# Performance work log

Hardware: AMD Instinct MI355X
Metric: run time of the kernel (lower is better)

Reference implementation:

```python
import jax, jax.numpy as jnp
import numpy as np

N_CARD = 100000
N_MERCH = 50000
E = 1000000
DIN = 64
H = 128


def setup_inputs() -> dict:
    key = jax.random.key(0)
    ks = iter(jax.random.split(key, 40))

    def nrm(shape, scale=0.05):
        return jax.random.normal(next(ks), shape, jnp.float32) * scale

    inp = {}
    inp["x_card"] = jax.random.normal(next(ks), (N_CARD, DIN), jnp.float32)
    inp["x_merchant"] = jax.random.normal(next(ks), (N_MERCH, DIN), jnp.float32)
    inp["src_cm"] = jax.random.randint(next(ks), (E,), 0, N_CARD, jnp.int32)
    inp["dst_cm"] = jax.random.randint(next(ks), (E,), 0, N_MERCH, jnp.int32)
    inp["src_mc"] = jax.random.randint(next(ks), (E,), 0, N_MERCH, jnp.int32)
    inp["dst_mc"] = jax.random.randint(next(ks), (E,), 0, N_CARD, jnp.int32)
    # SAGEConv weights per layer / edge type: lin_l (on aggregated msgs, with bias), lin_r (on dst, no bias)
    inp["Wl0_cm"] = nrm((DIN, H)); inp["bl0_cm"] = jnp.zeros((H,), jnp.float32); inp["Wr0_cm"] = nrm((DIN, H))
    inp["Wl0_mc"] = nrm((DIN, H)); inp["bl0_mc"] = jnp.zeros((H,), jnp.float32); inp["Wr0_mc"] = nrm((DIN, H))
    inp["Wl1_cm"] = nrm((H, H)); inp["bl1_cm"] = jnp.zeros((H,), jnp.float32); inp["Wr1_cm"] = nrm((H, H))
    inp["Wl1_mc"] = nrm((H, H)); inp["bl1_mc"] = jnp.zeros((H,), jnp.float32); inp["Wr1_mc"] = nrm((H, H))
    # per-node-type fraud classifiers: Linear(H, H//2) -> ReLU -> Linear(H//2, 2)
    inp["cW1_card"] = nrm((H, H // 2)); inp["cb1_card"] = jnp.zeros((H // 2,), jnp.float32)
    inp["cW2_card"] = nrm((H // 2, 2)); inp["cb2_card"] = jnp.zeros((2,), jnp.float32)
    inp["cW1_merch"] = nrm((H, H // 2)); inp["cb1_merch"] = jnp.zeros((H // 2,), jnp.float32)
    inp["cW2_merch"] = nrm((H // 2, 2)); inp["cb2_merch"] = jnp.zeros((2,), jnp.float32)
    # shared risk scorer: Linear(H, H//2) -> ReLU -> Linear(H//2, 1) -> sigmoid
    inp["rW1"] = nrm((H, H // 2)); inp["rb1"] = jnp.zeros((H // 2,), jnp.float32)
    inp["rW2"] = nrm((H // 2, 1)); inp["rb2"] = jnp.zeros((1,), jnp.float32)
    return inp


def _sage(x_src, x_dst, src, dst, Wl, bl, Wr, n_dst):
    # gather neighbor features, scatter-mean by destination, then lin_l + lin_r(x_dst)
    msg = x_src[src]                                           # [E, Din]
    agg = jax.ops.segment_sum(msg, dst, num_segments=n_dst)    # [n_dst, Din]
    cnt = jax.ops.segment_sum(jnp.ones((src.shape[0],), x_src.dtype), dst, num_segments=n_dst)
    mean = agg / jnp.maximum(cnt, 1.0)[:, None]
    return mean @ Wl + bl + x_dst @ Wr


def _mlp2(x, W1, b1, W2, b2):
    return jax.nn.relu(x @ W1 + b1) @ W2 + b2


def reference(x_card, x_merchant, src_cm, dst_cm, src_mc, dst_mc,
              Wl0_cm, bl0_cm, Wr0_cm, Wl0_mc, bl0_mc, Wr0_mc,
              Wl1_cm, bl1_cm, Wr1_cm, Wl1_mc, bl1_mc, Wr1_mc,
              cW1_card, cb1_card, cW2_card, cb2_card,
              cW1_merch, cb1_merch, cW2_merch, cb2_merch,
              rW1, rb1, rW2, rb2):
    # layer 0 (eval mode: dropout is identity)
    h_m = jax.nn.relu(_sage(x_card, x_merchant, src_cm, dst_cm, Wl0_cm, bl0_cm, Wr0_cm, N_MERCH))
    h_c = jax.nn.relu(_sage(x_merchant, x_card, src_mc, dst_mc, Wl0_mc, bl0_mc, Wr0_mc, N_CARD))
    # layer 1
    h_m2 = jax.nn.relu(_sage(h_c, h_m, src_cm, dst_cm, Wl1_cm, bl1_cm, Wr1_cm, N_MERCH))
    h_c2 = jax.nn.relu(_sage(h_m, h_c, src_mc, dst_mc, Wl1_mc, bl1_mc, Wr1_mc, N_CARD))
    # heads
    pred_c = _mlp2(h_c2, cW1_card, cb1_card, cW2_card, cb2_card)      # [N_CARD, 2]
    pred_m = _mlp2(h_m2, cW1_merch, cb1_merch, cW2_merch, cb2_merch)  # [N_MERCH, 2]
    risk_c = jax.nn.sigmoid(_mlp2(h_c2, rW1, rb1, rW2, rb2))[:, 0]    # [N_CARD]
    risk_m = jax.nn.sigmoid(_mlp2(h_m2, rW1, rb1, rW2, rb2))[:, 0]    # [N_MERCH]
    return (h_c2, h_m2, pred_c, pred_m, risk_c, risk_m)
```

## Files before the change

kernel.cpp:

```cpp
#include <hip/hip_runtime.h>


typedef unsigned short u16;
typedef unsigned int u32;
typedef short bf16x8 __attribute__((ext_vector_type(8)));
typedef float f32x4 __attribute__((ext_vector_type(4)));
typedef u16 u16x4 __attribute__((ext_vector_type(4)));
typedef u16 u16x8 __attribute__((ext_vector_type(8)));

#define CAP 64
#define LDS_PAD 8
#define NXCD 8
#define ECHUNK 64
#define NBUILD (NXCD * ECHUNK * 2)
#define NPACK  768

__device__ __forceinline__ float bf2f(u16 u) {
    union { u32 i; float f; } v; v.i = ((u32)u) << 16; return v.f;
}
__device__ __forceinline__ u16 f2bf(float f) {
    union { float f; u32 i; } v; v.f = f;
    u32 i = v.i;
    return (u16)((i + 0x7FFFu + ((i >> 16) & 1u)) >> 16);
}
__device__ __forceinline__ bf16x8 cvt8(const float* p) {
    bf16x8 r;
#pragma unroll
    for (int i = 0; i < 8; ++i) r[i] = (short)f2bf(p[i]);
    return r;
}

struct PackDesc { const float* src; u16* dst; int K; int Nsrc; int ntOff; };
struct PrepArgs {
    const int* src_cm; const int* dst_cm; const int* src_mc; const int* dst_mc;
    int* cnt_m; u32* bucket_m; int* cnt_c; u16* bucket_c;
    int E; int nMerch; int nCard;
    const float* xc; u16* xcb; int ncBlk;
    const float* xm; u16* xmb; int nmBlk;
    PackDesc pd[12];
};

__global__ void __launch_bounds__(256) prep(PrepArgs a) {
    const int b = blockIdx.x;
    if (b < NBUILD) {
        const int g = b & 7;
        const int chunk = (b >> 3) & 63;
        const bool dirA = b < (NBUILD / 2);
        const int nNode = dirA ? a.nMerch : a.nCard;
        const int lo = (int)((long long)g * nNode / NXCD);
        const int hi = (int)((long long)(g + 1) * nNode / NXCD);
        const int* dst = dirA ? a.dst_cm : a.dst_mc;
        const int* src = dirA ? a.src_cm : a.src_mc;
        int* cnt = dirA ? a.cnt_m : a.cnt_c;
        const int e0 = (int)((long long)chunk * a.E / ECHUNK);
        const int e1 = (int)((long long)(chunk + 1) * a.E / ECHUNK);
        for (int i = e0 + threadIdx.x; i < e1; i += 256) {
            int d = __builtin_nontemporal_load(dst + i);
            if (d >= lo && d < hi) {
                int slot = atomicAdd(&cnt[d], 1);
                if (slot < CAP) {
                    int s = __builtin_nontemporal_load(src + i);
                    if (dirA) a.bucket_m[(size_t)d * CAP + slot] = (u32)s;
                    else      a.bucket_c[(size_t)d * CAP + slot] = (u16)s;
                }
            }
        }
    } else if (b < NBUILD + NPACK) {
        int e = b - NBUILD;
        PackDesc pd = a.pd[e >> 6];
        int idx = (e & 63) * 256 + threadIdx.x;
        int j = idx & 7;
        int lane = (idx >> 3) & 63;
        int t = idx >> 9;
        int nLocal = pd.Nsrc >> 4;
        int ntl = t % nLocal;
        int kt = t / nLocal;
        if (kt >= (pd.K >> 5)) return;
        int k = kt * 32 + ((lane >> 4) << 3) + j;
        int n = ntl * 16 + (lane & 15);
        pd.dst[(((kt * 8 + pd.ntOff + ntl) * 64) + lane) * 8 + j] = f2bf(pd.src[k * pd.Nsrc + n]);
    } else {
        int e = b - NBUILD - NPACK;
        const float* s;
        u16* d;
        int n;
        if (e < a.ncBlk) { s = a.xc; d = a.xcb; n = a.nCard * 64; }
        else             { e -= a.ncBlk; s = a.xm; d = a.xmb; n = a.nMerch * 64; }
        int i = (e * 256 + threadIdx.x) * 4;
        if (i >= n) return;
        f32x4 v = *reinterpret_cast<const f32x4*>(s + i);
        u16x4 o;
#pragma unroll
        for (int j = 0; j < 4; ++j) o[j] = f2bf(v[j]);
        *reinterpret_cast<u16x4*>(d + i) = o;
    }
}

struct SageJob {
    const u16* src;
    const void* adj;
    const int* cnt;
    const u16* Wlp;
    const u16* dst;
    const u16* Wrp;
    const float* bias;
    float* outF;
    u16* outH;
    u16* outS;
    int M;
    int idx32;
    int nBlk;
};

template<int KF>
__global__ void __launch_bounds__(256) sage_pair(SageJob j0, SageJob j1) {
    constexpr int NV = KF / 16;
    __shared__ alignas(16) u16 lds[4][16][128 + LDS_PAD];
    const bool second = (int)blockIdx.x >= j0.nBlk;
    const SageJob& j = second ? j1 : j0;
    const int bx = second ? blockIdx.x - j0.nBlk : blockIdx.x;
    const int lane = threadIdx.x & 63;
    const int wv = threadIdx.x >> 6;
    const int m0 = (bx * 4 + wv) * 16;
    const bool active = (m0 < j.M);
    const int quad = lane >> 4;
    const int l15 = lane & 15;

    if (active) {
        const u16* srcH = j.src;
        const u32* adj32 = (const u32*)j.adj;
        const u16* adj16 = (const u16*)j.adj;
        const bool i32 = (j.idx32 != 0);
        int cv = j.cnt[m0 + l15];
        int cc_n = min(__shfl(cv, 0), CAP);
        int sidx_n = 0;
        if (lane < cc_n)
            sidx_n = i32 ? (int)adj32[(size_t)m0 * CAP + lane]
                         : (int)adj16[(size_t)m0 * CAP + lane];
        for (int r = 0; r < 16; ++r) {
            const int node = m0 + r;
            const int cc = cc_n;
            const int cfull = __shfl(cv, r);
            const int sidx = sidx_n;
            if (r < 15) {
                cc_n = min(__shfl(cv, r + 1), CAP);
                sidx_n = 0;
                if (lane < cc_n)
                    sidx_n = i32 ? (int)adj32[(size_t)(node + 1) * CAP + lane]
                                 : (int)adj16[(size_t)(node + 1) * CAP + lane];
            }
            float inv = 1.f / (float)max(cfull, 1);
            float acc0[NV], acc1[NV];
#pragma unroll
            for (int i = 0; i < NV; ++i) { acc0[i] = 0.f; acc1[i] = 0.f; }
            for (int t = 0; t < cc; t += 8) {
                int k0 = t + quad;
                int k1 = t + quad + 4;
                int s0 = __shfl(sidx, k0);
                int s1 = __shfl(sidx, k1);
                bool p0 = k0 < cc;
                bool p1 = k1 < cc;
                if constexpr (NV == 8) {
                    bf16x8 u0 = *(const bf16x8*)(srcH + (size_t)s0 * KF + l15 * 8);
                    bf16x8 u1 = *(const bf16x8*)(srcH + (size_t)s1 * KF + l15 * 8);
#pragma unroll
                    for (int i = 0; i < 8; ++i) {
                        acc0[i] += p0 ? bf2f((u16)u0[i]) : 0.f;
                        acc1[i] += p1 ? bf2f((u16)u1[i]) : 0.f;
                    }
                } else {
                    u16x4 u0 = *(const u16x4*)(srcH + (size_t)s0 * KF + l15 * 4);
                    u16x4 u1 = *(const u16x4*)(srcH + (size_t)s1 * KF + l15 * 4);
#pragma unroll
                    for (int i = 0; i < 4; ++i) {
                        acc0[i] += p0 ? bf2f(u0[i]) : 0.f;
                        acc1[i] += p1 ? bf2f(u1[i]) : 0.f;
                    }
                }
            }
            u16 packed[NV];
#pragma unroll
            for (int i = 0; i < NV; ++i) {
                float m = acc0[i] + acc1[i];
                m += __shfl_xor(m, 16);
                m += __shfl_xor(m, 32);
                packed[i] = f2bf(m * inv);
            }
            if (quad == 0) {
                if constexpr (NV == 8) *(u16x8*)&lds[wv][r][l15 * 8] = *(const u16x8*)packed;
                else                   *(u16x4*)&lds[wv][r][l15 * 4] = *(const u16x4*)packed;
            }
        }
    }
    __syncthreads();
    if (!active) return;

    constexpr int KT = KF >> 5;
    f32x4 acc[8];
#pragma unroll
    for (int i = 0; i < 8; ++i) acc[i] = (f32x4){0.f, 0.f, 0.f, 0.f};

#pragma unroll
    for (int kt = 0; kt < KT; ++kt) {
        bf16x8 a = *reinterpret_cast<const bf16x8*>(&lds[wv][l15][kt * 32 + quad * 8]);
#pragma unroll
        for (int nt = 0; nt < 8; ++nt) {
            bf16x8 bfr = *reinterpret_cast<const bf16x8*>(j.Wlp + (size_t)(((kt * 8 + nt) * 64 + lane) * 8));
            acc[nt] = __builtin_amdgcn_mfma_f32_16x16x32_bf16(a, bfr, acc[nt], 0, 0, 0);
        }
    }
#pragma unroll
    for (int kt = 0; kt < KT; ++kt) {
        bf16x8 a = *reinterpret_cast<const bf16x8*>(j.dst + (size_t)(m0 + l15) * KF + kt * 32 + quad * 8);
#pragma unroll
        for (int nt = 0; nt < 8; ++nt) {
            bf16x8 bfr = *reinterpret_cast<const bf16x8*>(j.Wrp + (size_t)(((kt * 8 + nt) * 64 + lane) * 8));
            acc[nt] = __builtin_amdgcn_mfma_f32_16x16x32_bf16(a, bfr, acc[nt], 0, 0, 0);
        }
    }
#pragma unroll
    for (int nt = 0; nt < 8; ++nt) {
        int col = nt * 16 + l15;
        float bv = j.bias[col];
#pragma unroll
        for (int r = 0; r < 4; ++r) {
            int row = m0 + quad * 4 + r;
            float v = fmaxf(acc[nt][r] + bv, 0.f);
            if (j.outF) j.outF[(size_t)row * 128 + col] = v;
            if (j.outH) j.outH[(size_t)row * 128 + col] = f2bf(v);
            if (j.outS) j.outS[(size_t)row * 128 + col] = f2bf(v);
        }
    }
}

template<typename IdxT, int KF, bool SRCF, bool DSTF, bool OUTF>
__global__ void __launch_bounds__(256) sage_fused(
    const void* __restrict__ Xsrc_, const IdxT* __restrict__ adj,
    const int* __restrict__ cnt,
    const u16* __restrict__ Wlp, const void* __restrict__ Xdst_,
    const u16* __restrict__ Wrp, const float* __restrict__ bias,
    void* __restrict__ out_, int M)
{
    constexpr int NV = KF / 16;
    __shared__ alignas(16) u16 lds[4][16][128 + LDS_PAD];
    const int lane = threadIdx.x & 63;
    const int wv = threadIdx.x >> 6;
    const int m0 = (blockIdx.x * 4 + wv) * 16;
    const bool active = (m0 < M);
    const int quad = lane >> 4;
    const int l15 = lane & 15;

    if (active) {
        const float* srcF = (const float*)Xsrc_;
        const u16*   srcH = (const u16*)Xsrc_;
        for (int r = 0; r < 16; ++r) {
            int node = m0 + r;
            int c = cnt[node];
            int cc = min(c, CAP);
            int sidx = (lane < cc) ? (int)adj[(size_t)node * CAP + lane] : 0;
            float inv = 1.f / (float)max(c, 1);
            float acc0[NV], acc1[NV];
#pragma unroll
            for (int i = 0; i < NV; ++i) { acc0[i] = 0.f; acc1[i] = 0.f; }
            for (int t = 0; t < cc; t += 8) {
                int k0 = t + quad, k1 = t + quad + 4;
                int s0 = __shfl(sidx, k0), s1 = __shfl(sidx, k1);
                bool p0 = k0 < cc, p1 = k1 < cc;
                if constexpr (SRCF) {
                    const f32x4* q0 = (const f32x4*)(srcF + (size_t)s0 * KF + l15 * NV);
                    const f32x4* q1 = (const f32x4*)(srcF + (size_t)s1 * KF + l15 * NV);
                    f32x4 u0 = q0[0], u1 = q1[0];
                    if constexpr (NV == 8) {
                        f32x4 w0 = q0[1], w1 = q1[1];
#pragma unroll
                        for (int i = 0; i < 4; ++i) {
                            acc0[4 + i] += p0 ? w0[i] : 0.f;
                            acc1[4 + i] += p1 ? w1[i] : 0.f;
                        }
                    }
#pragma unroll
                    for (int i = 0; i < 4; ++i) {
                        acc0[i] += p0 ? u0[i] : 0.f;
                        acc1[i] += p1 ? u1[i] : 0.f;
                    }
                } else {
                    if constexpr (NV == 8) {
                        bf16x8 u0 = *(const bf16x8*)(srcH + (size_t)s0 * KF + l15 * 8);
                        bf16x8 u1 = *(const bf16x8*)(srcH + (size_t)s1 * KF + l15 * 8);
#pragma unroll
                        for (int i = 0; i < 8; ++i) {
                            acc0[i] += p0 ? bf2f((u16)u0[i]) : 0.f;
                            acc1[i] += p1 ? bf2f((u16)u1[i]) : 0.f;
                        }
                    } else {
                        u16x4 u0 = *(const u16x4*)(srcH + (size_t)s0 * KF + l15 * 4);
                        u16x4 u1 = *(const u16x4*)(srcH + (size_t)s1 * KF + l15 * 4);
#pragma unroll
                        for (int i = 0; i < 4; ++i) {
                            acc0[i] += p0 ? bf2f(u0[i]) : 0.f;
                            acc1[i] += p1 ? bf2f(u1[i]) : 0.f;
                        }
                    }
                }
            }
            u16 packed[NV];
#pragma unroll
            for (int i = 0; i < NV; ++i) {
                float m = acc0[i] + acc1[i];
                m += __shfl_xor(m, 16);
                m += __shfl_xor(m, 32);
                packed[i] = f2bf(m * inv);
            }
            if (quad == 0) {
                if constexpr (NV == 8) *(u16x8*)&lds[wv][r][l15 * 8] = *(const u16x8*)packed;
                else                   *(u16x4*)&lds[wv][r][l15 * 4] = *(const u16x4*)packed;
            }
        }
    }
    __syncthreads();
    if (!active) return;

    constexpr int KT = KF >> 5;
    f32x4 acc[8];
#pragma unroll
    for (int i = 0; i < 8; ++i) acc[i] = (f32x4){0.f, 0.f, 0.f, 0.f};
#pragma unroll
    for (int kt = 0; kt < KT; ++kt) {
        bf16x8 a = *reinterpret_cast<const bf16x8*>(&lds[wv][l15][kt * 32 + quad * 8]);
#pragma unroll
        for (int nt = 0; nt < 8; ++nt) {
            bf16x8 b = *reinterpret_cast<const bf16x8*>(Wlp + (size_t)(((kt * 8 + nt) * 64 + lane) * 8));
            acc[nt] = __builtin_amdgcn_mfma_f32_16x16x32_bf16(a, b, acc[nt], 0, 0, 0);
        }
    }
#pragma unroll
    for (int kt = 0; kt < KT; ++kt) {
        bf16x8 a;
        if constexpr (DSTF) a = cvt8((const float*)Xdst_ + (size_t)(m0 + l15) * KF + kt * 32 + quad * 8);
        else                a = *reinterpret_cast<const bf16x8*>((const u16*)Xdst_ + (size_t)(m0 + l15) * KF + kt * 32 + quad * 8);
#pragma unroll
        for (int nt = 0; nt < 8; ++nt) {
            bf16x8 b = *reinterpret_cast<const bf16x8*>(Wrp + (size_t)(((kt * 8 + nt) * 64 + lane) * 8));
            acc[nt] = __builtin_amdgcn_mfma_f32_16x16x32_bf16(a, b, acc[nt], 0, 0, 0);
        }
    }
#pragma unroll
    for (int nt = 0; nt < 8; ++nt) {
        int col = nt * 16 + l15;
        float bv = bias[col];
#pragma unroll
        for (int r = 0; r < 4; ++r) {
            int row = m0 + quad * 4 + r;
            float v = fmaxf(acc[nt][r] + bv, 0.f);
            if constexpr (OUTF) ((float*)out_)[(size_t)row * 128 + col] = v;
            else                ((u16*)out_)[(size_t)row * 128 + col] = f2bf(v);
        }
    }
}

struct HeadJob {
    const float* X; const u16* W1p;
    const float* b1a; const float* b1b;
    const float* cW2; const float* cb2;
    const float* rW2; const float* rb2;
    float* pred; float* risk; int M; int nBlk;
};

__global__ void __launch_bounds__(256) head_pair(HeadJob h0, HeadJob h1) {
    __shared__ alignas(16) u16 lds[4][16][128 + LDS_PAD];
    const bool second = (int)blockIdx.x >= h0.nBlk;
    const HeadJob& h = second ? h1 : h0;
    const int bx = second ? blockIdx.x - h0.nBlk : blockIdx.x;
    const int lane = threadIdx.x & 63;
    const int wv = threadIdx.x >> 6;
    const int m0 = (bx * 4 + wv) * 16;
    const bool active = (m0 < h.M);
    const int quad = lane >> 4;
    const int l15 = lane & 15;

    if (active) {
        f32x4 acc[8];
#pragma unroll
        for (int i = 0; i < 8; ++i) acc[i] = (f32x4){0.f, 0.f, 0.f, 0.f};
#pragma unroll
        for (int kt = 0; kt < 4; ++kt) {
            bf16x8 a = cvt8(h.X + (size_t)(m0 + l15) * 128 + kt * 32 + quad * 8);
#pragma unroll
            for (int nt = 0; nt < 8; ++nt) {
                bf16x8 b = *reinterpret_cast<const bf16x8*>(h.W1p + (size_t)(((kt * 8 + nt) * 64 + lane) * 8));
                acc[nt] = __builtin_amdgcn_mfma_f32_16x16x32_bf16(a, b, acc[nt], 0, 0, 0);
            }
        }
#pragma unroll
        for (int nt = 0; nt < 8; ++nt) {
            int col = nt * 16 + l15;
            float bv = (col < 64) ? h.b1a[col] : h.b1b[col - 64];
#pragma unroll
            for (int r = 0; r < 4; ++r) {
                float v = fmaxf(acc[nt][r] + bv, 0.f);
                lds[wv][quad * 4 + r][col] = f2bf(v);
            }
        }
    }
    __syncthreads();
    if (!active) return;

    float w0 = h.cW2[lane * 2 + 0];
    float w1 = h.cW2[lane * 2 + 1];
    float w2 = h.rW2[lane];
    float cb0 = h.cb2[0], cb1v = h.cb2[1], rb = h.rb2[0];
    for (int r = 0; r < 16; ++r) {
        float t1 = bf2f(lds[wv][r][lane]);
        float t2 = bf2f(lds[wv][r][64 + lane]);
        float s0 = t1 * w0;
        float s1 = t1 * w1;
        float s2 = t2 * w2;
        for (int off = 32; off > 0; off >>= 1) {
            s0 += __shfl_xor(s0, off);
            s1 += __shfl_xor(s1, off);
            s2 += __shfl_xor(s2, off);
        }
        if (lane == 0) {
            int row = m0 + r;
            h.pred[(size_t)row * 2 + 0] = s0 + cb0;
            h.pred[(size_t)row * 2 + 1] = s1 + cb1v;
            float z = s2 + rb;
            h.risk[row] = 1.f / (1.f + __expf(-z));
        }
    }
}

#define OFF_CNT_M  ((size_t)0)
#define OFF_CNT_C  ((size_t)262144)
#define OFF_BKT_M  ((size_t)1  << 20)
#define OFF_BKT_C  ((size_t)14 << 20)
#define OFF_HM     ((size_t)27 << 20)
#define OFF_PACK   ((size_t)40 << 20)
#define OFF_XC     ((size_t)41 << 20)
#define OFF_XM     ((size_t)54 << 20)
#define OFF_HCB    ((size_t)61 << 20)
#define WS_SHADOW_NEED ((size_t)87 << 20)

extern "C" void kernel_launch(void* const* d_in, const int* in_sizes, int n_in,
                              void* d_out, int out_size, void* d_ws, size_t ws_size,
                              hipStream_t stream)
{
    const float* x_card   = (const float*)d_in[0];
    const float* x_merch  = (const float*)d_in[1];
    const int* src_cm     = (const int*)d_in[2];
    const int* dst_cm     = (const int*)d_in[3];
    const int* src_mc     = (const int*)d_in[4];
    const int* dst_mc     = (const int*)d_in[5];
    const float* Wl0_cm   = (const float*)d_in[6];
    const float* bl0_cm   = (const float*)d_in[7];
    const float* Wr0_cm   = (const float*)d_in[8];
    const float* Wl0_mc   = (const float*)d_in[9];
    const float* bl0_mc   = (const float*)d_in[10];
    const float* Wr0_mc   = (const float*)d_in[11];
    const float* Wl1_cm   = (const float*)d_in[12];
    const float* bl1_cm   = (const float*)d_in[13];
    const float* Wr1_cm   = (const float*)d_in[14];
    const float* Wl1_mc   = (const float*)d_in[15];
    const float* bl1_mc   = (const float*)d_in[16];
    const float* Wr1_mc   = (const float*)d_in[17];
    const float* cW1_card = (const float*)d_in[18];
    const float* cb1_card = (const float*)d_in[19];
    const float* cW2_card = (const float*)d_in[20];
    const float* cb2_card = (const float*)d_in[21];
    const float* cW1_mer  = (const float*)d_in[22];
    const float* cb1_mer  = (const float*)d_in[23];
    const float* cW2_mer  = (const float*)d_in[24];
    const float* cb2_mer  = (const float*)d_in[25];
    const float* rW1      = (const float*)d_in[26];
    const float* rb1      = (const float*)d_in[27];
    const float* rW2      = (const float*)d_in[28];
    const float* rb2      = (const float*)d_in[29];

    const int nCard  = in_sizes[0] / 64;
    const int nMerch = in_sizes[1] / 64;
    const int E      = in_sizes[2];

    char* ws = (char*)d_ws;
    int* cnt_m    = (int*)(ws + OFF_CNT_M);
    int* cnt_c    = (int*)(ws + OFF_CNT_C);
    u32* bucket_m = (u32*)(ws + OFF_BKT_M);
    u16* bucket_c = (u16*)(ws + OFF_BKT_C);
    u16* h_m      = (u16*)(ws + OFF_HM);
    u16* pw       = (u16*)(ws + OFF_PACK);
    u16* pWl0_cm = pw + 0 * 16384;
    u16* pWr0_cm = pw + 1 * 16384;
    u16* pWl0_mc = pw + 2 * 16384;
    u16* pWr0_mc = pw + 3 * 16384;
    u16* pWl1_cm = pw + 4 * 16384;
    u16* pWr1_cm = pw + 5 * 16384;
    u16* pWl1_mc = pw + 6 * 16384;
    u16* pWr1_mc = pw + 7 * 16384;
    u16* pHeadC  = pw + 8 * 16384;
    u16* pHeadM  = pw + 9 * 16384;
    u16* xc_bf   = (u16*)(ws + OFF_XC);
    u16* xm_bf   = (u16*)(ws + OFF_XM);
    u16* hc_bf   = (u16*)(ws + OFF_HCB);

    const bool shadow = (ws_size >= WS_SHADOW_NEED);

    float* out     = (float*)d_out;
    float* o_hc2   = out;
    float* o_hm2   = o_hc2 + (size_t)nCard * 128;
    float* o_predc = o_hm2 + (size_t)nMerch * 128;
    float* o_predm = o_predc + (size_t)nCard * 2;
    float* o_riskc = o_predm + (size_t)nMerch * 2;
    float* o_riskm = o_riskc + (size_t)nCard;

    hipMemsetAsync(ws, 0, OFF_CNT_C + (size_t)nCard * sizeof(int), stream);

    PrepArgs pa;
    pa.src_cm = src_cm; pa.dst_cm = dst_cm; pa.src_mc = src_mc; pa.dst_mc = dst_mc;
    pa.cnt_m = cnt_m; pa.bucket_m = bucket_m; pa.cnt_c = cnt_c; pa.bucket_c = bucket_c;
    pa.E = E; pa.nMerch = nMerch; pa.nCard = nCard;
    pa.xc = x_card;  pa.xcb = xc_bf; pa.ncBlk = shadow ? (nCard * 64 / 1024) : 0;
    pa.xm = x_merch; pa.xmb = xm_bf; pa.nmBlk = shadow ? (nMerch * 64 / 1024) : 0;
    pa.pd[0]  = { Wl0_cm,   pWl0_cm,  64, 128, 0 };
    pa.pd[1]  = { Wr0_cm,   pWr0_cm,  64, 128, 0 };
    pa.pd[2]  = { Wl0_mc,   pWl0_mc,  64, 128, 0 };
    pa.pd[3]  = { Wr0_mc,   pWr0_mc,  64, 128, 0 };
    pa.pd[4]  = { Wl1_cm,   pWl1_cm, 128, 128, 0 };
    pa.pd[5]  = { Wr1_cm,   pWr1_cm, 128, 128, 0 };
    pa.pd[6]  = { Wl1_mc,   pWl1_mc, 128, 128, 0 };
    pa.pd[7]  = { Wr1_mc,   pWr1_mc, 128, 128, 0 };
    pa.pd[8]  = { cW1_card, pHeadC,  128,  64, 0 };
    pa.pd[9]  = { rW1,      pHeadC,  128,  64, 4 };
    pa.pd[10] = { cW1_mer,  pHeadM,  128,  64, 0 };
    pa.pd[11] = { rW1,      pHeadM,  128,  64, 4 };
    int prepGrid = NBUILD + NPACK + pa.ncBlk + pa.nmBlk;
    prep<<<prepGrid, 256, 0, stream>>>(pa);

    const int nbM = (nMerch + 63) / 64;
    const int nbC = (nCard + 63) / 64;

    if (shadow) {
        SageJob a0 = { xc_bf, bucket_m, cnt_m, pWl0_cm, xm_bf, pWr0_cm, bl0_cm,
                       nullptr, h_m, nullptr, nMerch, 1, nbM };
        SageJob a1 = { xm_bf, bucket_c, cnt_c, pWl0_mc, xc_bf, pWr0_mc, bl0_mc,
                       o_hc2, nullptr, hc_bf, nCard, 0, nbC };
        sage_pair<64><<<nbM + nbC, 256, 0, stream>>>(a0, a1);

        SageJob b0 = { hc_bf, bucket_m, cnt_m, pWl1_cm, h_m, pWr1_cm, bl1_cm,
                       o_hm2, nullptr, nullptr, nMerch, 1, nbM };
        SageJob b1 = { h_m, bucket_c, cnt_c, pWl1_mc, hc_bf, pWr1_mc, bl1_mc,
                       o_hc2, nullptr, nullptr, nCard, 0, nbC };
        sage_pair<128><<<nbM + nbC, 256, 0, stream>>>(b0, b1);
    } else {
        sage_fused<u32, 64, true, true, false><<<nbM, 256, 0, stream>>>(
            x_card, bucket_m, cnt_m, pWl0_cm, x_merch, pWr0_cm, bl0_cm, h_m, nMerch);
        sage_fused<u16, 64, true, true, true><<<nbC, 256, 0, stream>>>(
            x_merch, bucket_c, cnt_c, pWl0_mc, x_card, pWr0_mc, bl0_mc, o_hc2, nCard);
        sage_fused<u32, 128, true, false, true><<<nbM, 256, 0, stream>>>(
            o_hc2, bucket_m, cnt_m, pWl1_cm, h_m, pWr1_cm, bl1_cm, o_hm2, nMerch);
        sage_fused<u16, 128, false, true, true><<<nbC, 256, 0, stream>>>(
            h_m, bucket_c, cnt_c, pWl1_mc, o_hc2, pWr1_mc, bl1_mc, o_hc2, nCard);
    }

    HeadJob hc = { o_hc2, pHeadC, cb1_card, rb1, cW2_card, cb2_card, rW2, rb2,
                   o_predc, o_riskc, nCard, nbC };
    HeadJob hm = { o_hm2, pHeadM, cb1_mer, rb1, cW2_mer, cb2_mer, rW2, rb2,
                   o_predm, o_riskm, nMerch, nbM };
    head_pair<<<nbC + nbM, 256, 0, stream>>>(hc, hm);
}
```

Measured before the change: 562.1 us.

## Fuse classifier heads into layer-1 SAGE kernel and widen neighbor gathers

Folds the prediction and risk MLP heads into the layer-1 sage_pair kernel. The layer-1 output goes through LDS straight into the head MFMA, which removes a separate head launch and the re-read of the fp32 layer outputs. The layer-0 kernel now gathers full 64-feature rows with 8 lanes per neighbor and 16 neighbors per step, and the layer-1 kernel processes two destination nodes per iteration to raise memory-level parallelism. Block-wide __syncthreads are replaced by early returns since each wave only uses its own LDS slice. The cost is more register pressure and larger kernel bodies.

```diff
diff --git a/kernel.cpp b/kernel.cpp
--- a/kernel.cpp
+++ b/kernel.cpp
@@ -110,11 +110,118 @@
     int M;
     int idx32;
     int nBlk;
+    const u16* hW1p;
+    const float* hb1a;
+    const float* hb1b;
+    const float* cW2; const float* cb2;
+    const float* rW2; const float* rb2;
+    float* pred; float* risk;
 };
 
-template<int KF>
-__global__ void __launch_bounds__(256) sage_pair(SageJob j0, SageJob j1) {
-    constexpr int NV = KF / 16;
+__global__ void __launch_bounds__(256) sage_pair64(SageJob j0, SageJob j1) {
+    __shared__ alignas(16) u16 lds[4][16][64 + LDS_PAD];
+    const bool second = (int)blockIdx.x >= j0.nBlk;
+    const SageJob& j = second ? j1 : j0;
+    const int bx = second ? blockIdx.x - j0.nBlk : blockIdx.x;
+    const int lane = threadIdx.x & 63;
+    const int wv = threadIdx.x >> 6;
+    const int m0 = (bx * 4 + wv) * 16;
+    if (m0 >= j.M) return;
+    const int quad = lane >> 4;
+    const int l15 = lane & 15;
+    const int nb8 = lane >> 3;
+    const int fl8 = lane & 7;
+
+    const u16* srcH = j.src;
+    const u32* adj32 = (const u32*)j.adj;
+    const u16* adj16 = (const u16*)j.adj;
+    const bool i32 = (j.idx32 != 0);
+
+    int cv = j.cnt[m0 + l15];
+    int cc_n = min(__shfl(cv, 0), CAP);
+    int sidx_n = 0;
+    if (lane < cc_n)
+        sidx_n = i32 ? (int)adj32[(size_t)m0 * CAP + lane]
+                     : (int)adj16[(size_t)m0 * CAP + lane];
+    for (int r = 0; r < 16; ++r) {
+        const int cc = cc_n;
+        const int cfull = __shfl(cv, r);
+        const int sidx = sidx_n;
+        if (r < 15) {
+            cc_n = min(__shfl(cv, r + 1), CAP);
+            sidx_n = 0;
+            if (lane < cc_n)
+                sidx_n = i32 ? (int)adj32[(size_t)(m0 + r + 1) * CAP + lane]
+                             : (int)adj16[(size_t)(m0 + r + 1) * CAP + lane];
+        }
+        float a0[8], a1[8];
+#pragma unroll
+        for (int i = 0; i < 8; ++i) { a0[i] = 0.f; a1[i] = 0.f; }
+        for (int t = 0; t < cc; t += 16) {
+            int k0 = t + nb8;
+            int k1 = t + nb8 + 8;
+            int s0 = __shfl(sidx, k0);
+            int s1 = __shfl(sidx, k1);
+            bool p0 = k0 < cc;
+            bool p1 = k1 < cc;
+            bf16x8 u0 = *(const bf16x8*)(srcH + (size_t)s0 * 64 + fl8 * 8);
+            bf16x8 u1 = *(const bf16x8*)(srcH + (size_t)s1 * 64 + fl8 * 8);
+#pragma unroll
+            for (int i = 0; i < 8; ++i) {
+                a0[i] += p0 ? bf2f((u16)u0[i]) : 0.f;
+                a1[i] += p1 ? bf2f((u16)u1[i]) : 0.f;
+            }
+        }
+        float inv = 1.f / (float)max(cfull, 1);
+        u16 packed[8];
+#pragma unroll
+        for (int i = 0; i < 8; ++i) {
+            float m = a0[i] + a1[i];
+            m += __shfl_xor(m, 8);
+            m += __shfl_xor(m, 16);
+            m += __shfl_xor(m, 32);
+            packed[i] = f2bf(m * inv);
+        }
+        if (nb8 == 0) *(u16x8*)&lds[wv][r][fl8 * 8] = *(const u16x8*)packed;
+    }
+
+    f32x4 acc[8];
+#pragma unroll
+    for (int i = 0; i < 8; ++i) acc[i] = (f32x4){0.f, 0.f, 0.f, 0.f};
+#pragma unroll
+    for (int kt = 0; kt < 2; ++kt) {
+        bf16x8 a = *reinterpret_cast<const bf16x8*>(&lds[wv][l15][kt * 32 + quad * 8]);
+#pragma unroll
+        for (int nt = 0; nt < 8; ++nt) {
+            bf16x8 b = *reinterpret_cast<const bf16x8*>(j.Wlp + (size_t)(((kt * 8 + nt) * 64 + lane) * 8));
+            acc[nt] = __builtin_amdgcn_mfma_f32_16x16x32_bf16(a, b, acc[nt], 0, 0, 0);
+        }
+    }
+#pragma unroll
+    for (int kt = 0; kt < 2; ++kt) {
+        bf16x8 a = *reinterpret_cast<const bf16x8*>(j.dst + (size_t)(m0 + l15) * 64 + kt * 32 + quad * 8);
+#pragma unroll
+        for (int nt = 0; nt < 8; ++nt) {
+            bf16x8 b = *reinterpret_cast<const bf16x8*>(j.Wrp + (size_t)(((kt * 8 + nt) * 64 + lane) * 8));
+            acc[nt] = __builtin_amdgcn_mfma_f32_16x16x32_bf16(a, b, acc[nt], 0, 0, 0);
+        }
+    }
+#pragma unroll
+    for (int nt = 0; nt < 8; ++nt) {
+        int col = nt * 16 + l15;
+        float bv = j.bias[col];
+#pragma unroll
+        for (int r = 0; r < 4; ++r) {
+            int row = m0 + quad * 4 + r;
+            float v = fmaxf(acc[nt][r] + bv, 0.f);
+            if (j.outF) j.outF[(size_t)row * 128 + col] = v;
+            if (j.outH) j.outH[(size_t)row * 128 + col] = f2bf(v);
+            if (j.outS) j.outS[(size_t)row * 128 + col] = f2bf(v);
+        }
+    }
+}
+
+__global__ void __launch_bounds__(256) sage_pair128(SageJob j0, SageJob j1) {
     __shared__ alignas(16) u16 lds[4][16][128 + LDS_PAD];
     const bool second = (int)blockIdx.x >= j0.nBlk;
     const SageJob& j = second ? j1 : j0;
@@ -122,100 +229,100 @@
     const int lane = threadIdx.x & 63;
     const int wv = threadIdx.x >> 6;
     const int m0 = (bx * 4 + wv) * 16;
-    const bool active = (m0 < j.M);
+    if (m0 >= j.M) return;
     const int quad = lane >> 4;
     const int l15 = lane & 15;
 
-    if (active) {
-        const u16* srcH = j.src;
-        const u32* adj32 = (const u32*)j.adj;
-        const u16* adj16 = (const u16*)j.adj;
-        const bool i32 = (j.idx32 != 0);
-        int cv = j.cnt[m0 + l15];
-        int cc_n = min(__shfl(cv, 0), CAP);
-        int sidx_n = 0;
-        if (lane < cc_n)
-            sidx_n = i32 ? (int)adj32[(size_t)m0 * CAP + lane]
-                         : (int)adj16[(size_t)m0 * CAP + lane];
-        for (int r = 0; r < 16; ++r) {
-            const int node = m0 + r;
-            const int cc = cc_n;
-            const int cfull = __shfl(cv, r);
-            const int sidx = sidx_n;
-            if (r < 15) {
-                cc_n = min(__shfl(cv, r + 1), CAP);
-                sidx_n = 0;
-                if (lane < cc_n)
-                    sidx_n = i32 ? (int)adj32[(size_t)(node + 1) * CAP + lane]
-                                 : (int)adj16[(size_t)(node + 1) * CAP + lane];
+    const u16* srcH = j.src;
+    const u32* adj32 = (const u32*)j.adj;
+    const u16* adj16 = (const u16*)j.adj;
+    const bool i32 = (j.idx32 != 0);
+
+    int cv = j.cnt[m0 + l15];
+    int ccA_n = min(__shfl(cv, 0), CAP);
+    int ccB_n = min(__shfl(cv, 1), CAP);
+    int sA_n = 0, sB_n = 0;
+    if (lane < ccA_n)
+        sA_n = i32 ? (int)adj32[(size_t)m0 * CAP + lane] : (int)adj16[(size_t)m0 * CAP + lane];
+    if (lane < ccB_n)
+        sB_n = i32 ? (int)adj32[(size_t)(m0 + 1) * CAP + lane] : (int)adj16[(size_t)(m0 + 1) * CAP + lane];
+
+    for (int r = 0; r < 16; r += 2) {
+        const int ccA = ccA_n, ccB = ccB_n;
+        const int sidxA = sA_n, sidxB = sB_n;
+        const int cfA = __shfl(cv, r);
+        const int cfB = __shfl(cv, r + 1);
+        if (r < 14) {
+            ccA_n = min(__shfl(cv, r + 2), CAP);
+            ccB_n = min(__shfl(cv, r + 3), CAP);
+            sA_n = 0; sB_n = 0;
+            if (lane < ccA_n)
+                sA_n = i32 ? (int)adj32[(size_t)(m0 + r + 2) * CAP + lane] : (int)adj16[(size_t)(m0 + r + 2) * CAP + lane];
+            if (lane < ccB_n)
+                sB_n = i32 ? (int)adj32[(size_t)(m0 + r + 3) * CAP + lane] : (int)adj16[(size_t)(m0 + r + 3) * CAP + lane];
+        }
+        float aA0[8], aA1[8], aB0[8], aB1[8];
+#pragma unroll
+        for (int i = 0; i < 8; ++i) { aA0[i] = 0.f; aA1[i] = 0.f; aB0[i] = 0.f; aB1[i] = 0.f; }
+        int cmax = max(ccA, ccB);
+        for (int t = 0; t < cmax; t += 8) {
+            int k0 = t + quad;
+            int k1 = t + quad + 4;
+            int sA0 = __shfl(sidxA, k0), sA1 = __shfl(sidxA, k1);
+            int sB0 = __shfl(sidxB, k0), sB1 = __shfl(sidxB, k1);
+            bool pA0 = k0 < ccA, pA1 = k1 < ccA;
+            bool pB0 = k0 < ccB, pB1 = k1 < ccB;
+            bf16x8 uA0 = *(const bf16x8*)(srcH + (size_t)sA0 * 128 + l15 * 8);
+            bf16x8 uA1 = *(const bf16x8*)(srcH + (size_t)sA1 * 128 + l15 * 8);
+            bf16x8 uB0 = *(const bf16x8*)(srcH + (size_t)sB0 * 128 + l15 * 8);
+            bf16x8 uB1 = *(const bf16x8*)(srcH + (size_t)sB1 * 128 + l15 * 8);
+#pragma unroll
+            for (int i = 0; i < 8; ++i) {
+                aA0[i] += pA0 ? bf2f((u16)uA0[i]) : 0.f;
+                aA1[i] += pA1 ? bf2f((u16)uA1[i]) : 0.f;
+                aB0[i] += pB0 ? bf2f((u16)uB0[i]) : 0.f;
+                aB1[i] += pB1 ? bf2f((u16)uB1[i]) : 0.f;
             }
-            float inv = 1.f / (float)max(cfull, 1);
-            float acc0[NV], acc1[NV];
-#pragma unroll
-            for (int i = 0; i < NV; ++i) { acc0[i] = 0.f; acc1[i] = 0.f; }
-            for (int t = 0; t < cc; t += 8) {
-                int k0 = t + quad;
-                int k1 = t + quad + 4;
-                int s0 = __shfl(sidx, k0);
-                int s1 = __shfl(sidx, k1);
-                bool p0 = k0 < cc;
-                bool p1 = k1 < cc;
-                if constexpr (NV == 8) {
-                    bf16x8 u0 = *(const bf16x8*)(srcH + (size_t)s0 * KF + l15 * 8);
-                    bf16x8 u1 = *(const bf16x8*)(srcH + (size_t)s1 * KF + l15 * 8);
-#pragma unroll
-                    for (int i = 0; i < 8; ++i) {
-                        acc0[i] += p0 ? bf2f((u16)u0[i]) : 0.f;
-                        acc1[i] += p1 ? bf2f((u16)u1[i]) : 0.f;
-                    }
-                } else {
-                    u16x4 u0 = *(const u16x4*)(srcH + (size_t)s0 * KF + l15 * 4);
-                    u16x4 u1 = *(const u16x4*)(srcH + (size_t)s1 * KF + l15 * 4);
-#pragma unroll
-                    for (int i = 0; i < 4; ++i) {
-                        acc0[i] += p0 ? bf2f(u0[i]) : 0.f;
-                        acc1[i] += p1 ? bf2f(u1[i]) : 0.f;
-                    }
-                }
-            }
-            u16 packed[NV];
-#pragma unroll
-            for (int i = 0; i < NV; ++i) {
-                float m = acc0[i] + acc1[i];
-                m += __shfl_xor(m, 16);
-                m += __shfl_xor(m, 32);
-                packed[i] = f2bf(m * inv);
-            }
-            if (quad == 0) {
-                if constexpr (NV == 8) *(u16x8*)&lds[wv][r][l15 * 8] = *(const u16x8*)packed;
-                else                   *(u16x4*)&lds[wv][r][l15 * 4] = *(const u16x4*)packed;
-            }
-        }
-    }
-    __syncthreads();
-    if (!active) return;
-
-    constexpr int KT = KF >> 5;
+        }
+        float invA = 1.f / (float)max(cfA, 1);
+        float invB = 1.f / (float)max(cfB, 1);
+        u16 pkA[8], pkB[8];
+#pragma unroll
+        for (int i = 0; i < 8; ++i) {
+            float mA = aA0[i] + aA1[i];
+            mA += __shfl_xor(mA, 16);
+            mA += __shfl_xor(mA, 32);
+            pkA[i] = f2bf(mA * invA);
+            float mB = aB0[i] + aB1[i];
+            mB += __shfl_xor(mB, 16);
+            mB += __shfl_xor(mB, 32);
+            pkB[i] = f2bf(mB * invB);
+        }
+        if (quad == 0) {
+            *(u16x8*)&lds[wv][r][l15 * 8] = *(const u16x8*)pkA;
+            *(u16x8*)&lds[wv][r + 1][l15 * 8] = *(const u16x8*)pkB;
+        }
+    }
+
     f32x4 acc[8];
 #pragma unroll
     for (int i = 0; i < 8; ++i) acc[i] = (f32x4){0.f, 0.f, 0.f, 0.f};
-
-#pragma unroll
-    for (int kt = 0; kt < KT; ++kt) {
+#pragma unroll
+    for (int kt = 0; kt < 4; ++kt) {
         bf16x8 a = *reinterpret_cast<const bf16x8*>(&lds[wv][l15][kt * 32 + quad * 8]);
 #pragma unroll
         for (int nt = 0; nt < 8; ++nt) {
-            bf16x8 bfr = *reinterpret_cast<const bf16x8*>(j.Wlp + (size_t)(((kt * 8 + nt) * 64 + lane) * 8));
-            acc[nt] = __builtin_amdgcn_mfma_f32_16x16x32_bf16(a, bfr, acc[nt], 0, 0, 0);
-        }
-    }
-#pragma unroll
-    for (int kt = 0; kt < KT; ++kt) {
-        bf16x8 a = *reinterpret_cast<const bf16x8*>(j.dst + (size_t)(m0 + l15) * KF + kt * 32 + quad * 8);
+            bf16x8 b = *reinterpret_cast<const bf16x8*>(j.Wlp + (size_t)(((kt * 8 + nt) * 64 + lane) * 8));
+            acc[nt] = __builtin_amdgcn_mfma_f32_16x16x32_bf16(a, b, acc[nt], 0, 0, 0);
+        }
+    }
+#pragma unroll
+    for (int kt = 0; kt < 4; ++kt) {
+        bf16x8 a = *reinterpret_cast<const bf16x8*>(j.dst + (size_t)(m0 + l15) * 128 + kt * 32 + quad * 8);
 #pragma unroll
         for (int nt = 0; nt < 8; ++nt) {
-            bf16x8 bfr = *reinterpret_cast<const bf16x8*>(j.Wrp + (size_t)(((kt * 8 + nt) * 64 + lane) * 8));
-            acc[nt] = __builtin_amdgcn_mfma_f32_16x16x32_bf16(a, bfr, acc[nt], 0, 0, 0);
+            bf16x8 b = *reinterpret_cast<const bf16x8*>(j.Wrp + (size_t)(((kt * 8 + nt) * 64 + lane) * 8));
+            acc[nt] = __builtin_amdgcn_mfma_f32_16x16x32_bf16(a, b, acc[nt], 0, 0, 0);
         }
     }
 #pragma unroll
@@ -227,8 +334,54 @@
             int row = m0 + quad * 4 + r;
             float v = fmaxf(acc[nt][r] + bv, 0.f);
             if (j.outF) j.outF[(size_t)row * 128 + col] = v;
-            if (j.outH) j.outH[(size_t)row * 128 + col] = f2bf(v);
-            if (j.outS) j.outS[(size_t)row * 128 + col] = f2bf(v);
+            lds[wv][quad * 4 + r][col] = f2bf(v);
+        }
+    }
+
+    if (!j.pred) return;
+    f32x4 hacc[8];
+#pragma unroll
+    for (int i = 0; i < 8; ++i) hacc[i] = (f32x4){0.f, 0.f, 0.f, 0.f};
+#pragma unroll
+    for (int kt = 0; kt < 4; ++kt) {
+        bf16x8 a = *reinterpret_cast<const bf16x8*>(&lds[wv][l15][kt * 32 + quad * 8]);
+#pragma unroll
+        for (int nt = 0; nt < 8; ++nt) {
+            bf16x8 b = *reinterpret_cast<const bf16x8*>(j.hW1p + (size_t)(((kt * 8 + nt) * 64 + lane) * 8));
+            hacc[nt] = __builtin_amdgcn_mfma_f32_16x16x32_bf16(a, b, hacc[nt], 0, 0, 0);
+        }
+    }
+#pragma unroll
+    for (int nt = 0; nt < 8; ++nt) {
+        int col = nt * 16 + l15;
+        float bv = (col < 64) ? j.hb1a[col] : j.hb1b[col - 64];
+#pragma unroll
+        for (int r = 0; r < 4; ++r) {
+            float v = fmaxf(hacc[nt][r] + bv, 0.f);
+            lds[wv][quad * 4 + r][col] = f2bf(v);
+        }
+    }
+    float w0 = j.cW2[lane * 2 + 0];
+    float w1 = j.cW2[lane * 2 + 1];
+    float w2 = j.rW2[lane];
+    float cb0 = j.cb2[0], cb1v = j.cb2[1], rb = j.rb2[0];
+    for (int r = 0; r < 16; ++r) {
+        float t1 = bf2f(lds[wv][r][lane]);
+        float t2 = bf2f(lds[wv][r][64 + lane]);
+        float s0 = t1 * w0;
+        float s1 = t1 * w1;
+        float s2 = t2 * w2;
+        for (int off = 32; off > 0; off >>= 1) {
+            s0 += __shfl_xor(s0, off);
+            s1 += __shfl_xor(s1, off);
+            s2 += __shfl_xor(s2, off);
+        }
+        if (lane == 0) {
+            int row = m0 + r;
+            j.pred[(size_t)row * 2 + 0] = s0 + cb0;
+            j.pred[(size_t)row * 2 + 1] = s1 + cb1v;
+            float z = s2 + rb;
+            j.risk[row] = 1.f / (1.f + __expf(-z));
         }
     }
 }
@@ -246,11 +399,11 @@
     const int lane = threadIdx.x & 63;
     const int wv = threadIdx.x >> 6;
     const int m0 = (blockIdx.x * 4 + wv) * 16;
-    const bool active = (m0 < M);
+    if (m0 >= M) return;
     const int quad = lane >> 4;
     const int l15 = lane & 15;
 
-    if (active) {
+    {
         const float* srcF = (const float*)Xsrc_;
         const u16*   srcH = (const u16*)Xsrc_;
         for (int r = 0; r < 16; ++r) {
@@ -317,8 +470,6 @@
             }
         }
     }
-    __syncthreads();
-    if (!active) return;
 
     constexpr int KT = KF >> 5;
     f32x4 acc[8];
@@ -374,36 +525,32 @@
     const int lane = threadIdx.x & 63;
     const int wv = threadIdx.x >> 6;
     const int m0 = (bx * 4 + wv) * 16;
-    const bool active = (m0 < h.M);
+    if (m0 >= h.M) return;
     const int quad = lane >> 4;
     const int l15 = lane & 15;
 
-    if (active) {
-        f32x4 acc[8];
-#pragma unroll
-        for (int i = 0; i < 8; ++i) acc[i] = (f32x4){0.f, 0.f, 0.f, 0.f};
-#pragma unroll
-        for (int kt = 0; kt < 4; ++kt) {
-            bf16x8 a = cvt8(h.X + (size_t)(m0 + l15) * 128 + kt * 32 + quad * 8);
-#pragma unroll
-            for (int nt = 0; nt < 8; ++nt) {
-                bf16x8 b = *reinterpret_cast<const bf16x8*>(h.W1p + (size_t)(((kt * 8 + nt) * 64 + lane) * 8));
-                acc[nt] = __builtin_amdgcn_mfma_f32_16x16x32_bf16(a, b, acc[nt], 0, 0, 0);
-            }
-        }
+    f32x4 acc[8];
+#pragma unroll
+    for (int i = 0; i < 8; ++i) acc[i] = (f32x4){0.f, 0.f, 0.f, 0.f};
+#pragma unroll
+    for (int kt = 0; kt < 4; ++kt) {
+        bf16x8 a = cvt8(h.X + (size_t)(m0 + l15) * 128 + kt * 32 + quad * 8);
 #pragma unroll
         for (int nt = 0; nt < 8; ++nt) {
-            int col = nt * 16 + l15;
-            float bv = (col < 64) ? h.b1a[col] : h.b1b[col - 64];
-#pragma unroll
-            for (int r = 0; r < 4; ++r) {
-                float v = fmaxf(acc[nt][r] + bv, 0.f);
-                lds[wv][quad * 4 + r][col] = f2bf(v);
-            }
-        }
-    }
-    __syncthreads();
-    if (!active) return;
+            bf16x8 b = *reinterpret_cast<const bf16x8*>(h.W1p + (size_t)(((kt * 8 + nt) * 64 + lane) * 8));
+            acc[nt] = __builtin_amdgcn_mfma_f32_16x16x32_bf16(a, b, acc[nt], 0, 0, 0);
+        }
+    }
+#pragma unroll
+    for (int nt = 0; nt < 8; ++nt) {
+        int col = nt * 16 + l15;
+        float bv = (col < 64) ? h.b1a[col] : h.b1b[col - 64];
+#pragma unroll
+        for (int r = 0; r < 4; ++r) {
+            float v = fmaxf(acc[nt][r] + bv, 0.f);
+            lds[wv][quad * 4 + r][col] = f2bf(v);
+        }
+    }
 
     float w0 = h.cW2[lane * 2 + 0];
     float w1 = h.cW2[lane * 2 + 1];
@@ -539,16 +686,24 @@
 
     if (shadow) {
         SageJob a0 = { xc_bf, bucket_m, cnt_m, pWl0_cm, xm_bf, pWr0_cm, bl0_cm,
-                       nullptr, h_m, nullptr, nMerch, 1, nbM };
+                       nullptr, h_m, nullptr, nMerch, 1, nbM,
+                       nullptr, nullptr, nullptr, nullptr, nullptr, nullptr, nullptr,
+                       nullptr, nullptr };
         SageJob a1 = { xm_bf, bucket_c, cnt_c, pWl0_mc, xc_bf, pWr0_mc, bl0_mc,
-                       o_hc2, nullptr, hc_bf, nCard, 0, nbC };
-        sage_pair<64><<<nbM + nbC, 256, 0, stream>>>(a0, a1);
+                       o_hc2, nullptr, hc_bf, nCard, 0, nbC,
+                       nullptr, nullptr, nullptr, nullptr, nullptr, nullptr, nullptr,
+                       nullptr, nullptr };
+        sage_pair64<<<nbM + nbC, 256, 0, stream>>>(a0, a1);
 
         SageJob b0 = { hc_bf, bucket_m, cnt_m, pWl1_cm, h_m, pWr1_cm, bl1_cm,
-                       o_hm2, nullptr, nullptr, nMerch, 1, nbM };
+                       o_hm2, nullptr, nullptr, nMerch, 1, nbM,
+                       pHeadM, cb1_mer, rb1, cW2_mer, cb2_mer, rW2, rb2,
+                       o_predm, o_riskm };
         SageJob b1 = { h_m, bucket_c, cnt_c, pWl1_mc, hc_bf, pWr1_mc, bl1_mc,
-                       o_hc2, nullptr, nullptr, nCard, 0, nbC };
-        sage_pair<128><<<nbM + nbC, 256, 0, stream>>>(b0, b1);
+                       o_hc2, nullptr, nullptr, nCard, 0, nbC,
+                       pHeadC, cb1_card, rb1, cW2_card, cb2_card, rW2, rb2,
+                       o_predc, o_riskc };
+        sage_pair128<<<nbM + nbC, 256, 0, stream>>>(b0, b1);
     } else {
         sage_fused<u32, 64, true, true, false><<<nbM, 256, 0, stream>>>(
             x_card, bucket_m, cnt_m, pWl0_cm, x_merch, pWr0_cm, bl0_cm, h_m, nMerch);
@@ -558,11 +713,10 @@
             o_hc2, bucket_m, cnt_m, pWl1_cm, h_m, pWr1_cm, bl1_cm, o_hm2, nMerch);
         sage_fused<u16, 128, false, true, true><<<nbC, 256, 0, stream>>>(
             h_m, bucket_c, cnt_c, pWl1_mc, o_hc2, pWr1_mc, bl1_mc, o_hc2, nCard);
-    }
-
-    HeadJob hc = { o_hc2, pHeadC, cb1_card, rb1, cW2_card, cb2_card, rW2, rb2,
-                   o_predc, o_riskc, nCard, nbC };
-    HeadJob hm = { o_hm2, pHeadM, cb1_mer, rb1, cW2_mer, cb2_mer, rW2, rb2,
-                   o_predm, o_riskm, nMerch, nbM };
-    head_pair<<<nbC + nbM, 256, 0, stream>>>(hc, hm);
-}
+        HeadJob hc = { o_hc2, pHeadC, cb1_card, rb1, cW2_card, cb2_card, rW2, rb2,
+                       o_predc, o_riskc, nCard, nbC };
+        HeadJob hm = { o_hm2, pHeadM, cb1_mer, rb1, cW2_mer, cb2_mer, rW2, rb2,
+                       o_predm, o_riskm, nMerch, nbM };
+        head_pair<<<nbC + nbM, 256, 0, stream>>>(hc, hm);
+    }
+}
```

Result: slower. 575.8 us (+2.4%).
